# Kernel tuning notes

Measured on AMD Instinct MI355X. Metric: run time of the kernel, lower is better.

Reference implementation:

```python
import jax, jax.numpy as jnp
import numpy as np
from jax import lax

B, C, Dd, Hh, Ww = 2, 256, 8, 64, 64
E, HID, TOPK = 6, 1024, 3


def setup_inputs() -> dict:
    key = jax.random.key(0)
    ks = jax.random.split(key, 8)
    return {
        "x": jax.random.normal(ks[0], (B, C, Dd, Hh, Ww), jnp.float32),
        "attention_weights": jax.random.uniform(ks[1], (B, Dd, Hh, Ww), jnp.float32),
        "gate_w": jax.random.normal(ks[2], (E, C), jnp.float32) * 0.02,
        "gate_b": jnp.zeros((E,), jnp.float32),
        "w1": jax.random.normal(ks[3], (E, HID, C), jnp.float32) * (1.0 / np.sqrt(C)),
        "b1": jnp.zeros((E, HID), jnp.float32),
        "w2": jax.random.normal(ks[4], (E, C, HID), jnp.float32) * (1.0 / np.sqrt(HID)),
        "b2": jnp.zeros((E, C), jnp.float32),
    }


def reference(x, attention_weights, gate_w, gate_b, w1, b1, w2, b2):
    b, c, d, h, w = x.shape
    n = d * h * w
    e = gate_w.shape[0]
    xt = x.reshape(b, c, n).transpose(0, 2, 1)  # [B, N, C] tokens
    # 1x1x1 gate conv == per-voxel linear
    gv = jnp.einsum('bnc,ec->bne', xt, gate_w) + gate_b  # [B, N, E]
    gv = gv * attention_weights.reshape(b, n, 1)
    gv = jax.nn.softmax(gv, axis=-1)  # softmax over experts (dim=1 in torch layout)
    top_v, top_i = lax.top_k(gv, TOPK)  # [B, N, 3]
    # scatter top-k softmax values into a zero mask (non-topk experts get 0)
    mask = jnp.sum(jax.nn.one_hot(top_i, e, dtype=gv.dtype) * top_v[..., None], axis=-2)  # [B, N, E]
    out = jnp.zeros_like(xt)
    for ei in range(e):  # loop over small fixed expert count
        hdn = jax.nn.gelu(jnp.einsum('bnc,hc->bnh', xt, w1[ei]) + b1[ei], approximate=False)
        o = jnp.einsum('bnh,ch->bnc', hdn, w2[ei]) + b2[ei]
        out = out + mask[:, :, ei:ei + 1] * o
    return out.transpose(0, 2, 1).reshape(b, c, d, h, w)
```

## Files before the change

kernel.cpp:

```cpp
#include <hip/hip_runtime.h>
#include <hip/hip_bf16.h>
#include <math.h>

#define NN 32768
#define CC 256
#define EE 6
#define HID 1024
#define TT 64
#define NTOK 65536
#define NTILE_MAX 1044
#define NT3MAX 3078
#define NT3MAX2 1548
#define SENT 0xFFFFFFFFu

typedef __attribute__((ext_vector_type(8))) short bf16x8;
typedef __attribute__((ext_vector_type(4))) float f32x4;
typedef __attribute__((ext_vector_type(4))) unsigned int u32x4;
typedef __attribute__((ext_vector_type(2))) unsigned int u32x2;

__device__ const int CMB[20][3] = {
  {0,1,2},{0,1,3},{0,1,4},{0,1,5},{0,2,3},{0,2,4},{0,2,5},{0,3,4},{0,3,5},{0,4,5},
  {1,2,3},{1,2,4},{1,2,5},{1,3,4},{1,3,5},{1,4,5},{2,3,4},{2,3,5},{2,4,5},{3,4,5}};
__device__ const unsigned char M2B[64] = {
  255,255,255,255,255,255,255,  0,
  255,255,255,  1,255,  4, 10,255,
  255,255,255,  2,255,  5, 11,255,
  255,  7, 13,255, 16,255,255,255,
  255,255,255,  3,255,  6, 12,255,
  255,  8, 14,255, 17,255,255,255,
  255,  9, 15,255, 18,255,255,255,
   19,255,255,255,255,255,255,255};

__device__ __forceinline__ unsigned short f32_bf16(float f) {
  unsigned u = __builtin_bit_cast(unsigned, f);
  u += 0x7FFFu + ((u >> 16) & 1u);
  return (unsigned short)(u >> 16);
}

__device__ __forceinline__ unsigned cvt_pk_bf16(float lo, float hi) {
  unsigned r;
  asm("v_cvt_pk_bf16_f32 %0, %1, %2" : "=v"(r) : "v"(lo), "v"(hi));
  return r;
}

__device__ __forceinline__ float fast_gelu(float v) {
  float s = v * v;
  float a = v * -2.3021181819f;
  float m = a * 0.044715f;
  float nu = __builtin_fmaf(m, s, a);
  float z = __builtin_amdgcn_exp2f(nu);
  return v * __builtin_amdgcn_rcpf(1.0f + z);
}

__global__ void wconv(const float* __restrict__ w1, const float* __restrict__ w2,
                      unsigned short* __restrict__ w1b, unsigned short* __restrict__ w2b) {
  int i = blockIdx.x * 256 + threadIdx.x;
  w1b[i] = f32_bf16(w1[i]);
  w2b[i] = f32_bf16(w2[i]);
}


__global__ __launch_bounds__(256) void gatepack_k(
    const float* __restrict__ x, const float* __restrict__ attn,
    const float* __restrict__ gate_w, const float* __restrict__ gate_b,
    unsigned* __restrict__ setid, float* __restrict__ wsel,
    unsigned* __restrict__ ehist, unsigned char* __restrict__ Xp3) {
  __shared__ float gws[EE * CC];
  __shared__ unsigned char lx[TT * 512];
  __shared__ float gred[256 * EE];
  __shared__ unsigned hist6[EE];

  const int tid = threadIdx.x, lane = tid & 63, wv = tid >> 6;
  const int n0g = blockIdx.x * TT;
  const int bI = n0g >> 15, n0 = n0g & (NN - 1);

  for (int i = tid; i < EE * CC; i += 256) gws[i] = gate_w[i];
  if (tid < EE) hist6[tid] = 0;
  __syncthreads();

  {
    float gp[EE] = {0.f, 0.f, 0.f, 0.f, 0.f, 0.f};
    const size_t xbase = ((size_t)bI * CC + wv * 64) * NN + n0 + lane;
    #pragma unroll 1
    for (int c8 = 0; c8 < 8; ++c8) {
      float xv[8];
      #pragma unroll
      for (int j = 0; j < 8; ++j)
        xv[j] = x[xbase + (size_t)(c8 * 8 + j) * NN];
      #pragma unroll
      for (int j = 0; j < 8; ++j) {
        int c = wv * 64 + c8 * 8 + j;
        #pragma unroll
        for (int e = 0; e < EE; ++e) gp[e] = __builtin_fmaf(xv[j], gws[e * CC + c], gp[e]);
      }
      u32x4 pk;
      #pragma unroll
      for (int q = 0; q < 4; ++q) pk[q] = cvt_pk_bf16(xv[2 * q], xv[2 * q + 1]);
      *(u32x4*)(lx + lane * 512 + (wv * 64 + c8 * 8) * 2) = pk;
    }
    #pragma unroll
    for (int e = 0; e < EE; ++e) gred[(wv * 64 + lane) * EE + e] = gp[e];
  }
  __syncthreads();

  if (tid < 64) {
    float g[EE];
    #pragma unroll
    for (int e = 0; e < EE; ++e)
      g[e] = gred[(0 * 64 + tid) * EE + e] + gred[(1 * 64 + tid) * EE + e] +
             gred[(2 * 64 + tid) * EE + e] + gred[(3 * 64 + tid) * EE + e];
    float aw = attn[n0g + tid];
    float m = -1e30f;
    #pragma unroll
    for (int e = 0; e < EE; ++e) { g[e] = (g[e] + gate_b[e]) * aw; m = fmaxf(m, g[e]); }
    float ex[EE], s = 0.f;
    #pragma unroll
    for (int e = 0; e < EE; ++e) { ex[e] = expf(g[e] - m); s += ex[e]; }
    int i1 = 0; float v1 = g[0];
    #pragma unroll
    for (int e = 1; e < EE; ++e) if (g[e] > v1) { v1 = g[e]; i1 = e; }
    int i2 = -1; float v2 = -3.4e38f;
    #pragma unroll
    for (int e = 0; e < EE; ++e) if (e != i1 && g[e] > v2) { v2 = g[e]; i2 = e; }
    int i3 = -1; float v3 = -3.4e38f;
    #pragma unroll
    for (int e = 0; e < EE; ++e) if (e != i1 && e != i2 && g[e] > v3) { v3 = g[e]; i3 = e; }
    const unsigned msk = (1u << i1) | (1u << i2) | (1u << i3);
    float inv = 1.f / s;
    int slot = 0;
    #pragma unroll
    for (int e = 0; e < EE; ++e)
      if ((msk >> e) & 1u) wsel[(size_t)(n0g + tid) * 3 + (slot++)] = ex[e] * inv;
    setid[n0g + tid] = (unsigned)M2B[msk];
    atomicAdd(&hist6[i1], 1u); atomicAdd(&hist6[i2], 1u); atomicAdd(&hist6[i3], 1u);
  }
  __syncthreads();

  #pragma unroll 1
  for (int r = 0; r < 16; ++r) {
    const int t = wv * 16 + r;
    u32x2 v = *(const u32x2*)(lx + t * 512 + lane * 8);
    *(u32x2*)(Xp3 + (size_t)(n0g + t) * 512 + lane * 8) = v;
  }
  if (tid < EE) ehist[tid * 1024 + blockIdx.x] = hist6[tid];
}

__global__ __launch_bounds__(256) void prefix3_k(
    const unsigned* __restrict__ ehist, unsigned* __restrict__ ebase,
    unsigned* __restrict__ desc3, unsigned* __restrict__ tlist3,
    float* __restrict__ wp3) {
  __shared__ unsigned sc[256];
  __shared__ unsigned tot[EE], bb[EE + 1], grp[EE], tcum[EE + 1];
  const int tid = threadIdx.x;
  #pragma unroll 1
  for (int e = 0; e < EE; ++e) {
    unsigned v[4]; unsigned s = 0;
    #pragma unroll
    for (int k = 0; k < 4; ++k) { v[k] = ehist[e * 1024 + tid * 4 + k]; s += v[k]; }
    sc[tid] = s; __syncthreads();
    for (int off = 1; off < 256; off <<= 1) {
      unsigned tv = (tid >= off) ? sc[tid - off] : 0u; __syncthreads();
      sc[tid] += tv; __syncthreads();
    }
    unsigned excl = sc[tid] - s;
    if (tid == 255) tot[e] = sc[255];
    unsigned run = excl;
    #pragma unroll
    for (int k = 0; k < 4; ++k) { ebase[e * 1024 + tid * 4 + k] = run; run += v[k]; }
    __syncthreads();
  }
  if (tid == 0) {
    unsigned base = 0, tc = 0;
    for (int e = 0; e < EE; ++e) {
      bb[e] = base; tcum[e] = tc;
      unsigned gl = (tot[e] + 63) >> 6;
      grp[e] = gl;
      tc += (gl + 1) >> 1;
      base += gl << 6;
    }
    bb[EE] = base; tcum[EE] = tc;
  }
  __syncthreads();
  #pragma unroll 1
  for (int e = 0; e < EE; ++e) {
    unsigned b0 = bb[e];
    #pragma unroll
    for (int k = 0; k < 4; ++k) ebase[e * 1024 + tid * 4 + k] += b0;
  }
  if (tid < EE) {
    for (unsigned i = bb[tid] + tot[tid]; i < bb[tid + 1]; ++i) {
      tlist3[i] = SENT; wp3[i] = 0.f;
    }
  }
  __syncthreads();
  const unsigned nt = tcum[EE];
  for (int i = tid; i < NT3MAX2; i += 256) {
    unsigned d;
    if ((unsigned)i < nt) {
      int e = 0;
      while (!((unsigned)i >= tcum[e] && (unsigned)i < tcum[e + 1])) ++e;
      unsigned li = (unsigned)i - tcum[e];
      unsigned g = (bb[e] >> 6) + 2u * li;
      unsigned nh = (2u * li + 1u < grp[e]) ? 1u : 0u;
      d = ((unsigned)e << 20) | (nh << 19) | g;
    } else d = 0x3Fu << 20;
    desc3[i] = d;
  }
}

__global__ __launch_bounds__(64) void scatter3_k(
    const unsigned* __restrict__ setid, const unsigned* __restrict__ ebase,
    const float* __restrict__ wsel,
    unsigned* __restrict__ tlist3, float* __restrict__ wp3, unsigned* __restrict__ pos3) {
  const int tid = threadIdx.x;
  const int blk = blockIdx.x;
  const unsigned id = blk * 64 + tid;
  const unsigned bkt = setid[id];
  const unsigned m6 =
      (1u << CMB[bkt][0]) | (1u << CMB[bkt][1]) | (1u << CMB[bkt][2]);
  const unsigned long long below = (1ull << tid) - 1ull;
  int s = 0;
  #pragma unroll
  for (int e = 0; e < EE; ++e) {
    unsigned long long bl = __ballot((m6 >> e) & 1u);
    if ((m6 >> e) & 1u) {
      unsigned rank = (unsigned)__builtin_popcountll(bl & below);
      unsigned p = ebase[e * 1024 + blk] + rank;
      tlist3[p] = id;
      wp3[p] = wsel[(size_t)id * 3 + s];
      pos3[(size_t)id * 3 + s] = p;
      s++;
    }
  }
}

__global__ __launch_bounds__(512, 2) void moe_main3(
    const float* __restrict__ b1, const float* __restrict__ b2,
    const unsigned short* __restrict__ w1b, const unsigned short* __restrict__ w2b,
    const unsigned* __restrict__ desc3, const unsigned* __restrict__ tlist3,
    const float* __restrict__ wp3, const unsigned char* __restrict__ Xp3,
    unsigned char* __restrict__ Op3) {
  __shared__ unsigned char xs[128 * 512];
  __shared__ unsigned char hs[128 * 512];
  __shared__ unsigned tokS[128];
  __shared__ float w3S[128];

  const unsigned d = desc3[blockIdx.x];
  const unsigned e = d >> 20;
  if (e > 5) return;
  const int nh = (int)((d >> 19) & 1u);
  const int lstart = (int)(d & 0x7FFFFu) << 6;

  const int tid  = threadIdx.x;
  const int lane = tid & 63;
  const int wv   = tid >> 6;
  const int lr   = lane & 15;
  const int lg   = lane >> 4;

  if (tid < 128) {
    const int valid = (tid < 64) | nh;
    tokS[tid] = valid ? tlist3[lstart + tid] : SENT;
    w3S[tid]  = valid ? wp3[lstart + tid] : 0.f;
  }
  __syncthreads();

  {
    const int t = tid >> 2, q = tid & 3;
    unsigned tk = tokS[t];
    if (tk == SENT) tk = 0u;
    const unsigned char* src = Xp3 + (size_t)tk * 512 + q * 128;
    const unsigned tsw = ((unsigned)(t & 31)) << 4;
    #pragma unroll
    for (int i = 0; i < 8; ++i) {
      u32x4 v = *(const u32x4*)(src + i * 16);
      *(u32x4*)(xs + t * 512 + (((unsigned)(q * 128 + i * 16)) ^ tsw)) = v;
    }
  }
  __syncthreads();

  f32x4 oacc[2][8];
  #pragma unroll
  for (int fm = 0; fm < 2; ++fm)
    #pragma unroll
    for (int fn = 0; fn < 8; ++fn) oacc[fm][fn] = (f32x4){0.f, 0.f, 0.f, 0.f};

  unsigned trowA[8], tswA[8];
  #pragma unroll
  for (int fn = 0; fn < 8; ++fn) {
    int t = fn * 16 + lr;
    trowA[fn] = (unsigned)t * 512u;
    tswA[fn]  = ((unsigned)(t & 31)) << 4;
  }

  const unsigned short* w1base =
      w1b + ((size_t)(e * HID + wv * 32 + lr)) * CC + lg * 8;
  const unsigned short* w2base =
      w2b + ((size_t)(e * CC + wv * 32 + lr)) * HID + lg * 8;

  #pragma unroll 1
  for (int sc = 0; sc < 4; ++sc) {
    const unsigned short* w1c = w1base + (size_t)(sc * 256) * CC;
    const unsigned short* w2c = w2base + sc * 256;

    f32x4 hacc[2][8];
    #pragma unroll
    for (int fm = 0; fm < 2; ++fm)
      #pragma unroll
      for (int fn = 0; fn < 8; ++fn) hacc[fm][fn] = (f32x4){0.f, 0.f, 0.f, 0.f};
    #pragma unroll
    for (int ks = 0; ks < 8; ++ks) {
      bf16x8 af[2], bx[8];
      #pragma unroll
      for (int fm = 0; fm < 2; ++fm)
        af[fm] = *(const bf16x8*)(w1c + fm * 16 * CC + ks * 32);
      #pragma unroll
      for (int fn = 0; fn < 8; ++fn)
        bx[fn] = *(const bf16x8*)(xs + trowA[fn] +
                                  (((unsigned)(ks * 64 + lg * 16)) ^ tswA[fn]));
      #pragma unroll
      for (int fn = 0; fn < 8; ++fn)
        #pragma unroll
        for (int fm = 0; fm < 2; ++fm)
          hacc[fm][fn] =
              __builtin_amdgcn_mfma_f32_16x16x32_bf16(af[fm], bx[fn], hacc[fm][fn], 0, 0, 0);
    }

    {
      f32x4 b1v[2];
      #pragma unroll
      for (int fm = 0; fm < 2; ++fm)
        b1v[fm] = *(const f32x4*)&b1[e * HID + sc * 256 + wv * 32 + fm * 16 + lg * 4];
      #pragma unroll
      for (int fn = 0; fn < 8; ++fn) {
        float msk = w3S[fn * 16 + lr];
        #pragma unroll
        for (int fm = 0; fm < 2; ++fm) {
          float gg[4];
          #pragma unroll
          for (int r = 0; r < 4; ++r)
            gg[r] = fast_gelu(hacc[fm][fn][r] + b1v[fm][r]) * msk;
          u32x2 pk;
          pk[0] = cvt_pk_bf16(gg[0], gg[1]);
          pk[1] = cvt_pk_bf16(gg[2], gg[3]);
          unsigned byteo = trowA[fn] +
              (((unsigned)((wv * 32 + fm * 16 + lg * 4) * 2)) ^ tswA[fn]);
          *(u32x2*)(hs + byteo) = pk;
        }
      }
    }
    __syncthreads();

    #pragma unroll
    for (int ks = 0; ks < 8; ++ks) {
      bf16x8 am[2], bh[8];
      #pragma unroll
      for (int fm = 0; fm < 2; ++fm)
        am[fm] = *(const bf16x8*)(w2c + fm * 16 * HID + ks * 32);
      #pragma unroll
      for (int fn = 0; fn < 8; ++fn)
        bh[fn] = *(const bf16x8*)(hs + trowA[fn] +
                                  (((unsigned)(ks * 64 + lg * 16)) ^ tswA[fn]));
      #pragma unroll
      for (int fn = 0; fn < 8; ++fn)
        #pragma unroll
        for (int fm = 0; fm < 2; ++fm)
          oacc[fm][fn] =
              __builtin_amdgcn_mfma_f32_16x16x32_bf16(am[fm], bh[fn], oacc[fm][fn], 0, 0, 0);
    }
    __syncthreads();
  }

  float wt[8];
  #pragma unroll
  for (int fn = 0; fn < 8; ++fn) wt[fn] = w3S[fn * 16 + lr];
  #pragma unroll
  for (int fm = 0; fm < 2; ++fm) {
    f32x4 b2v = *(const f32x4*)&b2[e * CC + wv * 32 + fm * 16 + lg * 4];
    #pragma unroll
    for (int fn = 0; fn < 8; ++fn)
      #pragma unroll
      for (int r = 0; r < 4; ++r)
        oacc[fm][fn][r] = __builtin_fmaf(wt[fn], b2v[r], oacc[fm][fn][r]);
  }
  #pragma unroll
  for (int fn = 0; fn < 8; ++fn) {
    if (fn >= 4 && !nh) continue;
    const int row = lstart + fn * 16 + lr;
    unsigned char* po = Op3 + (size_t)row * 512;
    #pragma unroll
    for (int fm = 0; fm < 2; ++fm) {
      u32x2 pk;
      pk[0] = cvt_pk_bf16(oacc[fm][fn][0], oacc[fm][fn][1]);
      pk[1] = cvt_pk_bf16(oacc[fm][fn][2], oacc[fm][fn][3]);
      *(u32x2*)(po + (wv * 32 + fm * 16 + lg * 4) * 2) = pk;
    }
  }
}

__global__ __launch_bounds__(256) void unscatter3_k(
    const unsigned char* __restrict__ Op3, const unsigned* __restrict__ pos3,
    float* __restrict__ out) {
  __shared__ float lo[32 * 261];
  __shared__ unsigned psf[96];
  const int tid = threadIdx.x;
  const int n0g = blockIdx.x * 32;
  const int b = n0g >> 15, n0 = n0g & (NN - 1);

  if (tid < 96) psf[tid] = pos3[(size_t)n0g * 3 + tid];
  __syncthreads();

  #pragma unroll
  for (int j = 0; j < 8; ++j) {
    const int row = j * 4 + (tid >> 6);
    const int c = (tid & 63) * 4;
    float a0 = 0.f, a1 = 0.f, a2 = 0.f, a3 = 0.f;
    #pragma unroll
    for (int s = 0; s < 3; ++s) {
      const unsigned r = psf[row * 3 + s];
      u32x2 v = *(const u32x2*)(Op3 + (size_t)r * 512 + c * 2);
      a0 += __builtin_bit_cast(float, v[0] << 16);
      a1 += __builtin_bit_cast(float, v[0] & 0xFFFF0000u);
      a2 += __builtin_bit_cast(float, v[1] << 16);
      a3 += __builtin_bit_cast(float, v[1] & 0xFFFF0000u);
    }
    lo[row * 261 + c + 0] = a0; lo[row * 261 + c + 1] = a1;
    lo[row * 261 + c + 2] = a2; lo[row * 261 + c + 3] = a3;
  }
  __syncthreads();

  const int noff = tid & 31, cq = tid >> 5;
  float* po = out + (size_t)b * CC * NN + n0 + noff;
  #pragma unroll
  for (int j2 = 0; j2 < 32; ++j2) {
    int c = cq * 32 + j2;
    po[(size_t)c * NN] = lo[noff * 261 + c];
  }
}


__global__ __launch_bounds__(256) void gate_k(
    const float* __restrict__ x, const float* __restrict__ attn,
    const float* __restrict__ gate_w, const float* __restrict__ gate_b,
    unsigned* __restrict__ setid, float* __restrict__ wsel,
    unsigned* __restrict__ bhist) {
  __shared__ float gws[EE * CC];
  __shared__ unsigned hist[20];
  const int tid = threadIdx.x;
  const int blk = blockIdx.x;
  for (int i = tid; i < EE * CC; i += 256) gws[i] = gate_w[i];
  if (tid < 20) hist[tid] = 0;
  __syncthreads();

  const unsigned id = blk * 256 + tid;
  const int b = id >> 15, n = id & (NN - 1);
  const float* px = x + (size_t)b * CC * NN + n;
  float g[EE] = {0.f, 0.f, 0.f, 0.f, 0.f, 0.f};
  #pragma unroll 4
  for (int c = 0; c < CC; ++c) {
    float xv = px[(size_t)c * NN];
    #pragma unroll
    for (int e = 0; e < EE; ++e) g[e] = __builtin_fmaf(xv, gws[e * CC + c], g[e]);
  }
  float aw = attn[id];
  float m = -1e30f;
  #pragma unroll
  for (int e = 0; e < EE; ++e) { g[e] = (g[e] + gate_b[e]) * aw; m = fmaxf(m, g[e]); }
  float ex[EE], s = 0.f;
  #pragma unroll
  for (int e = 0; e < EE; ++e) { ex[e] = expf(g[e] - m); s += ex[e]; }
  int i1 = 0; float v1 = g[0];
  #pragma unroll
  for (int e = 1; e < EE; ++e) if (g[e] > v1) { v1 = g[e]; i1 = e; }
  int i2 = -1; float v2 = -3.4e38f;
  #pragma unroll
  for (int e = 0; e < EE; ++e) if (e != i1 && g[e] > v2) { v2 = g[e]; i2 = e; }
  int i3 = -1; float v3 = -3.4e38f;
  #pragma unroll
  for (int e = 0; e < EE; ++e) if (e != i1 && e != i2 && g[e] > v3) { v3 = g[e]; i3 = e; }
  const unsigned msk = (1u << i1) | (1u << i2) | (1u << i3);
  const unsigned bkt = M2B[msk];
  float inv = 1.f / s;
  int slot = 0;
  #pragma unroll
  for (int e = 0; e < EE; ++e)
    if ((msk >> e) & 1u) wsel[(size_t)id * 3 + (slot++)] = ex[e] * inv;
  setid[id] = bkt;
  atomicAdd(&hist[bkt], 1u);
  __syncthreads();
  if (tid < 20) bhist[blk * 20 + tid] = hist[tid];
}

__global__ void prefix_k(const unsigned* __restrict__ bhist, unsigned* __restrict__ bbase,
                         unsigned* __restrict__ desc) {
  __shared__ unsigned tot[20];
  __shared__ unsigned bb[21];
  __shared__ unsigned tcum[21];
  const int tid = threadIdx.x;
  if (tid < 20) {
    unsigned run = 0;
    for (int blk = 0; blk < 256; ++blk) {
      unsigned v = bhist[blk * 20 + tid];
      bbase[blk * 20 + tid] = run;
      run += v;
    }
    tot[tid] = run;
  }
  __syncthreads();
  if (tid == 0) {
    unsigned base = 0, tc = 0;
    for (int b = 0; b < 20; ++b) {
      bb[b] = base; tcum[b] = tc;
      unsigned tl = (tot[b] + 63) >> 6;
      tc += tl; base += tl << 6;
    }
    bb[20] = base; tcum[20] = tc;
  }
  __syncthreads();
  if (tid < 20) {
    unsigned b0 = bb[tid];
    for (int blk = 0; blk < 256; ++blk) bbase[blk * 20 + tid] += b0;
  }
  __syncthreads();
  const unsigned nt = tcum[20];
  for (int i = tid; i < NTILE_MAX; i += 256) {
    unsigned d;
    if ((unsigned)i < nt) {
      int b = 0;
      while (!((unsigned)i >= tcum[b] && (unsigned)i < tcum[b + 1])) ++b;
      d = ((unsigned)b << 16) | ((bb[b] >> 6) + ((unsigned)i - tcum[b]));
    } else {
      d = 0x003F0000u;
    }
    desc[i] = d;
  }
}

__global__ __launch_bounds__(256) void scatter_k(
    const unsigned* __restrict__ setid, const unsigned* __restrict__ bbase,
    const float* __restrict__ wsel,
    unsigned* __restrict__ pos, float* __restrict__ wp) {
  __shared__ unsigned wcnt[4][20];
  const int tid = threadIdx.x, lane = tid & 63, w = tid >> 6;
  const int blk = blockIdx.x;
  const unsigned id = blk * 256 + tid;
  const unsigned sid = setid[id];
  unsigned long long myb = 0;
  #pragma unroll
  for (int b = 0; b < 20; ++b) {
    unsigned long long bl = __ballot(sid == (unsigned)b);
    if (lane == 0) wcnt[w][b] = (unsigned)__builtin_popcountll(bl);
    if ((unsigned)b == sid) myb = bl;
  }
  __syncthreads();
  unsigned rank = 0;
  #pragma unroll
  for (int w2 = 0; w2 < 4; ++w2) if (w2 < w) rank += wcnt[w2][sid];
  rank += (unsigned)__builtin_popcountll(myb & ((1ull << lane) - 1ull));
  const unsigned p = bbase[blk * 20 + sid] + rank;
  pos[id] = p;
  #pragma unroll
  for (int s = 0; s < 3; ++s) wp[(size_t)p * 3 + s] = wsel[(size_t)id * 3 + s];
}

__global__ __launch_bounds__(256) void xpack_k(
    const float* __restrict__ x, const unsigned* __restrict__ pos,
    unsigned char* __restrict__ Xp) {
  __shared__ unsigned char lx[TT * 512];
  __shared__ unsigned posS[TT];
  const int tid = threadIdx.x, lane = tid & 63, wv = tid >> 6;
  const int n0g = blockIdx.x * TT;
  const int b = n0g >> 15, n0 = n0g & (NN - 1);

  if (tid < TT) posS[tid] = pos[n0g + tid];

  const float* px = x + (size_t)b * CC * NN + n0 + lane;
  #pragma unroll 1
  for (int c8 = 0; c8 < 8; ++c8) {
    float xv[8];
    #pragma unroll
    for (int j = 0; j < 8; ++j)
      xv[j] = px[(size_t)(wv * 64 + c8 * 8 + j) * NN];
    u32x4 pk;
    #pragma unroll
    for (int q = 0; q < 4; ++q) pk[q] = cvt_pk_bf16(xv[2 * q], xv[2 * q + 1]);
    *(u32x4*)(lx + lane * 512 + (wv * 64 + c8 * 8) * 2) = pk;
  }
  __syncthreads();

  #pragma unroll 1
  for (int r = 0; r < 16; ++r) {
    const int t = wv * 16 + r;
    const unsigned p = posS[t];
    u32x2 v = *(const u32x2*)(lx + t * 512 + lane * 8);
    *(u32x2*)(Xp + (size_t)p * 512 + (((unsigned)(lane * 8)) ^ (((unsigned)(p & 31)) << 4))) = v;
  }
}

__global__ __launch_bounds__(256, 2) void moe_main(
    const float* __restrict__ b1, const float* __restrict__ b2,
    const unsigned short* __restrict__ w1b, const unsigned short* __restrict__ w2b,
    const unsigned* __restrict__ desc, const float* __restrict__ wp,
    const unsigned char* __restrict__ Xp, float* __restrict__ Op) {
  __shared__ unsigned char xs[TT * CC * 2];
  __shared__ unsigned char hs[TT * 256 * 2];
  __shared__ float w3S[3 * TT];

  const unsigned d = desc[blockIdx.x];
  const unsigned bkt = d >> 16;
  if (bkt > 19) return;
  const int lstart = (int)(d & 0xFFFFu) << 6;

  const int tid  = threadIdx.x;
  const int lane = tid & 63;
  const int wv   = tid >> 6;
  const int lr   = lane & 15;
  const int lg   = lane >> 4;

  if (tid < 3 * TT) {
    int t = tid & 63, s = tid >> 6;
    w3S[s * 64 + t] = wp[(size_t)(lstart + t) * 3 + s];
  }

  {
    const unsigned char* src = Xp + (size_t)lstart * 512;
    #pragma unroll
    for (int it = 0; it < 8; ++it) {
      u32x4 v = *(const u32x4*)(src + it * 4096 + tid * 16);
      *(u32x4*)(xs + it * 4096 + tid * 16) = v;
    }
  }
  __syncthreads();

  f32x4 oacc[4][4];
  #pragma unroll
  for (int fm = 0; fm < 4; ++fm)
    #pragma unroll
    for (int fn = 0; fn < 4; ++fn) oacc[fm][fn] = (f32x4){0.f, 0.f, 0.f, 0.f};

  unsigned trowA[4], tswA[4];
  #pragma unroll
  for (int fn = 0; fn < 4; ++fn) {
    int t = fn * 16 + lr;
    trowA[fn] = (unsigned)t * 512u;
    tswA[fn]  = ((unsigned)(t & 31)) << 4;
  }

  #pragma unroll 1
  for (int xe = 0; xe < 3; ++xe) {
    const int e = CMB[bkt][xe];
    #pragma unroll 1
    for (int sc = 0; sc < 4; ++sc) {
      f32x4 hacc[4][4];
      #pragma unroll
      for (int fm = 0; fm < 4; ++fm)
        #pragma unroll
        for (int fn = 0; fn < 4; ++fn) hacc[fm][fn] = (f32x4){0.f, 0.f, 0.f, 0.f};
      const unsigned short* w1p =
          w1b + ((size_t)(e * HID + sc * 256 + wv * 64 + lr)) * CC + lg * 8;
      #pragma unroll
      for (int ks = 0; ks < 8; ++ks) {
        bf16x8 af[4], bx[4];
        #pragma unroll
        for (int fm = 0; fm < 4; ++fm)
          af[fm] = *(const bf16x8*)(w1p + fm * 16 * CC + ks * 32);
        #pragma unroll
        for (int fn = 0; fn < 4; ++fn)
          bx[fn] = *(const bf16x8*)(xs + trowA[fn] +
                                    (((unsigned)(ks * 64 + lg * 16)) ^ tswA[fn]));
        #pragma unroll
        for (int fn = 0; fn < 4; ++fn)
          #pragma unroll
          for (int fm = 0; fm < 4; ++fm)
            hacc[fm][fn] =
                __builtin_amdgcn_mfma_f32_16x16x32_bf16(af[fm], bx[fn], hacc[fm][fn], 0, 0, 0);
      }
      {
        f32x4 b1v[4];
        #pragma unroll
        for (int fm = 0; fm < 4; ++fm)
          b1v[fm] = *(const f32x4*)&b1[e * HID + sc * 256 + wv * 64 + fm * 16 + lg * 4];
        #pragma unroll
        for (int fn = 0; fn < 4; ++fn) {
          float msk = w3S[xe * 64 + fn * 16 + lr];
          #pragma unroll
          for (int fm = 0; fm < 4; ++fm) {
            float gg[4];
            #pragma unroll
            for (int r = 0; r < 4; ++r)
              gg[r] = fast_gelu(hacc[fm][fn][r] + b1v[fm][r]) * msk;
            u32x2 pk;
            pk[0] = cvt_pk_bf16(gg[0], gg[1]);
            pk[1] = cvt_pk_bf16(gg[2], gg[3]);
            unsigned byteo = trowA[fn] +
                (((unsigned)((wv * 64 + fm * 16 + lg * 4) * 2)) ^ tswA[fn]);
            *(u32x2*)(hs + byteo) = pk;
          }
        }
      }
      __syncthreads();
      const unsigned short* w2p =
          w2b + ((size_t)(e * CC + wv * 64 + lr)) * HID + sc * 256 + lg * 8;
      #pragma unroll
      for (int ks = 0; ks < 8; ++ks) {
        bf16x8 am[4], bh[4];
        #pragma unroll
        for (int fm = 0; fm < 4; ++fm)
          am[fm] = *(const bf16x8*)(w2p + fm * 16 * HID + ks * 32);
        #pragma unroll
        for (int fn = 0; fn < 4; ++fn)
          bh[fn] = *(const bf16x8*)(hs + trowA[fn] +
                                    (((unsigned)(ks * 64 + lg * 16)) ^ tswA[fn]));
        #pragma unroll
        for (int fn = 0; fn < 4; ++fn)
          #pragma unroll
          for (int fm = 0; fm < 4; ++fm)
            oacc[fm][fn] =
                __builtin_amdgcn_mfma_f32_16x16x32_bf16(am[fm], bh[fn], oacc[fm][fn], 0, 0, 0);
      }
      __syncthreads();
    }
  }

  #pragma unroll
  for (int xe = 0; xe < 3; ++xe) {
    const int e = CMB[bkt][xe];
    float msk[4];
    #pragma unroll
    for (int fn = 0; fn < 4; ++fn) msk[fn] = w3S[xe * 64 + fn * 16 + lr];
    #pragma unroll
    for (int fm = 0; fm < 4; ++fm) {
      f32x4 b2v = *(const f32x4*)&b2[e * CC + wv * 64 + fm * 16 + lg * 4];
      #pragma unroll
      for (int fn = 0; fn < 4; ++fn)
        #pragma unroll
        for (int r = 0; r < 4; ++r)
          oacc[fm][fn][r] = __builtin_fmaf(msk[fn], b2v[r], oacc[fm][fn][r]);
    }
  }
  #pragma unroll
  for (int fn = 0; fn < 4; ++fn) {
    float* po = Op + (size_t)(lstart + fn * 16 + lr) * CC;
    #pragma unroll
    for (int fm = 0; fm < 4; ++fm)
      *(f32x4*)(po + wv * 64 + fm * 16 + lg * 4) = oacc[fm][fn];
  }
}

__global__ __launch_bounds__(256) void unscatter_k(
    const float* __restrict__ Op, const unsigned* __restrict__ pos,
    float* __restrict__ out) {
  __shared__ float lo[32 * 261];
  __shared__ unsigned posS[32];
  const int tid = threadIdx.x;
  const int n0g = blockIdx.x * 32;
  const int b = n0g >> 15, n0 = n0g & (NN - 1);

  if (tid < 32) posS[tid] = pos[n0g + tid];
  __syncthreads();

  #pragma unroll
  for (int j = 0; j < 8; ++j) {
    int fidx = j * 1024 + tid * 4;
    int row = fidx >> 8, c = fidx & 255;
    f32x4 v = *(const f32x4*)(Op + (size_t)posS[row] * CC + c);
    #pragma unroll
    for (int i = 0; i < 4; ++i) lo[row * 261 + c + i] = v[i];
  }
  __syncthreads();

  const int noff = tid & 31, cq = tid >> 5;
  float* po = out + (size_t)b * CC * NN + n0 + noff;
  #pragma unroll
  for (int j2 = 0; j2 < 32; ++j2) {
    int c = cq * 32 + j2;
    po[(size_t)c * NN] = lo[noff * 261 + c];
  }
}


extern "C" void kernel_launch(void* const* d_in, const int* in_sizes, int n_in,
                              void* d_out, int out_size, void* d_ws, size_t ws_size,
                              hipStream_t stream) {
  const float* x      = (const float*)d_in[0];
  const float* attn   = (const float*)d_in[1];
  const float* gate_w = (const float*)d_in[2];
  const float* gate_b = (const float*)d_in[3];
  const float* w1     = (const float*)d_in[4];
  const float* b1     = (const float*)d_in[5];
  const float* w2     = (const float*)d_in[6];
  const float* b2     = (const float*)d_in[7];
  float* out = (float*)d_out;

  unsigned char* ws = (unsigned char*)d_ws;
  unsigned short* w1b  = (unsigned short*)(ws);
  unsigned short* w2b  = (unsigned short*)(ws + 3145728);
  unsigned*       setid= (unsigned*)(ws + 6291456);
  float*          wsel = (float*)(ws + 6553600);
  unsigned*       bhist= (unsigned*)(ws + 7340032);
  unsigned*       bbase= (unsigned*)(ws + 7360512);
  unsigned*       desc = (unsigned*)(ws + 7381120);
  unsigned*       pos  = (unsigned*)(ws + 7385344);
  float*          wp   = (float*)(ws + 7647488);
  unsigned char*  Xp   = (unsigned char*)(ws + 8449280);
  float*          Op   = (float*)(ws + 42659072);
  const size_t need_bucket = 111078656;
  unsigned*       ehist = (unsigned*)(ws + 7360512);
  unsigned*       ebase = (unsigned*)(ws + 7385088);
  unsigned*       desc3 = (unsigned*)(ws + 7409664);
  unsigned*       tlist3= (unsigned*)(ws + 7422208);
  float*          wp3   = (float*)(ws + 8210176);
  unsigned*       pos3  = (unsigned*)(ws + 8998144);
  unsigned char*  Xp3   = (unsigned char*)(ws + 9784576);
  unsigned char*  Op3   = (unsigned char*)(ws + 43339008);
  const size_t need3 = 144198912;

  wconv<<<(EE * HID * CC) / 256, 256, 0, stream>>>(w1, w2, w1b, w2b);
  if (ws_size >= need3) {
    gatepack_k<<<NTOK / TT, 256, 0, stream>>>(x, attn, gate_w, gate_b, setid, wsel, ehist, Xp3);
    prefix3_k<<<1, 256, 0, stream>>>(ehist, ebase, desc3, tlist3, wp3);
    scatter3_k<<<NTOK / 64, 64, 0, stream>>>(setid, ebase, wsel, tlist3, wp3, pos3);
    moe_main3<<<NT3MAX2, 512, 0, stream>>>(b1, b2, w1b, w2b, desc3, tlist3, wp3, Xp3, Op3);
    unscatter3_k<<<NTOK / 32, 256, 0, stream>>>(Op3, pos3, out);
  } else {
    gate_k<<<NTOK / 256, 256, 0, stream>>>(x, attn, gate_w, gate_b, setid, wsel, bhist);
    prefix_k<<<1, 256, 0, stream>>>(bhist, bbase, desc);
    scatter_k<<<NTOK / 256, 256, 0, stream>>>(setid, bbase, wsel, pos, wp);
    xpack_k<<<NTOK / TT, 256, 0, stream>>>(x, pos, Xp);
    moe_main<<<NTILE_MAX, 256, 0, stream>>>(b1, b2, w1b, w2b, desc, wp, Xp, Op);
    unscatter_k<<<NTOK / 32, 256, 0, stream>>>(Op, pos, out);
  }
}
```

Measured before the change: 522.7 us.

## Repartition MoE expert kernel so each wave owns 16 tokens end-to-end

```diff
diff --git a/kernel.cpp b/kernel.cpp
--- a/kernel.cpp
+++ b/kernel.cpp
@@ -241,7 +241,7 @@
     const float* __restrict__ wp3, const unsigned char* __restrict__ Xp3,
     unsigned char* __restrict__ Op3) {
   __shared__ unsigned char xs[128 * 512];
-  __shared__ unsigned char hs[128 * 512];
+  __shared__ unsigned char hs[8 * 8192];
   __shared__ unsigned tokS[128];
   __shared__ float w3S[128];
 
@@ -278,122 +278,89 @@
   }
   __syncthreads();
 
-  f32x4 oacc[2][8];
-  #pragma unroll
-  for (int fm = 0; fm < 2; ++fm)
-    #pragma unroll
-    for (int fn = 0; fn < 8; ++fn) oacc[fm][fn] = (f32x4){0.f, 0.f, 0.f, 0.f};
-
-  unsigned trowA[8], tswA[8];
-  #pragma unroll
-  for (int fn = 0; fn < 8; ++fn) {
-    int t = fn * 16 + lr;
-    trowA[fn] = (unsigned)t * 512u;
-    tswA[fn]  = ((unsigned)(t & 31)) << 4;
-  }
-
-  const unsigned short* w1base =
-      w1b + ((size_t)(e * HID + wv * 32 + lr)) * CC + lg * 8;
-  const unsigned short* w2base =
-      w2b + ((size_t)(e * CC + wv * 32 + lr)) * HID + lg * 8;
+  if (wv >= 4 && !nh) return;
+
+  const int myt = wv * 16 + lr;
+  const float msk = w3S[myt];
+  unsigned char* hw = hs + wv * 8192 + lr * 512;
+  const unsigned swz8 = ((unsigned)(lr & 7)) << 4;
+
+  bf16x8 bx[8];
+  {
+    const unsigned char* xrow = xs + myt * 512;
+    const unsigned tsw = ((unsigned)(myt & 31)) << 4;
+    #pragma unroll
+    for (int ks = 0; ks < 8; ++ks)
+      bx[ks] = *(const bf16x8*)(xrow + (((unsigned)(ks * 64 + lg * 16)) ^ tsw));
+  }
+
+  f32x4 oacc[16];
+  #pragma unroll
+  for (int cf = 0; cf < 16; ++cf) oacc[cf] = (f32x4){0.f, 0.f, 0.f, 0.f};
+
+  const unsigned short* w1base = w1b + ((size_t)(e * HID) + lr) * CC + lg * 8;
+  const unsigned short* w2base = w2b + ((size_t)(e * CC) + lr) * HID + lg * 8;
 
   #pragma unroll 1
   for (int sc = 0; sc < 4; ++sc) {
-    const unsigned short* w1c = w1base + (size_t)(sc * 256) * CC;
-    const unsigned short* w2c = w2base + sc * 256;
-
-    f32x4 hacc[2][8];
-    #pragma unroll
-    for (int fm = 0; fm < 2; ++fm)
-      #pragma unroll
-      for (int fn = 0; fn < 8; ++fn) hacc[fm][fn] = (f32x4){0.f, 0.f, 0.f, 0.f};
-    #pragma unroll
-    for (int ks = 0; ks < 8; ++ks) {
-      bf16x8 af[2], bx[8];
-      #pragma unroll
-      for (int fm = 0; fm < 2; ++fm)
-        af[fm] = *(const bf16x8*)(w1c + fm * 16 * CC + ks * 32);
-      #pragma unroll
-      for (int fn = 0; fn < 8; ++fn)
-        bx[fn] = *(const bf16x8*)(xs + trowA[fn] +
-                                  (((unsigned)(ks * 64 + lg * 16)) ^ tswA[fn]));
-      #pragma unroll
-      for (int fn = 0; fn < 8; ++fn)
-        #pragma unroll
-        for (int fm = 0; fm < 2; ++fm)
-          hacc[fm][fn] =
-              __builtin_amdgcn_mfma_f32_16x16x32_bf16(af[fm], bx[fn], hacc[fm][fn], 0, 0, 0);
-    }
-
+    f32x4 hacc[16];
+    #pragma unroll
+    for (int hf = 0; hf < 16; ++hf) hacc[hf] = (f32x4){0.f, 0.f, 0.f, 0.f};
     {
-      f32x4 b1v[2];
-      #pragma unroll
-      for (int fm = 0; fm < 2; ++fm)
-        b1v[fm] = *(const f32x4*)&b1[e * HID + sc * 256 + wv * 32 + fm * 16 + lg * 4];
-      #pragma unroll
-      for (int fn = 0; fn < 8; ++fn) {
-        float msk = w3S[fn * 16 + lr];
-        #pragma unroll
-        for (int fm = 0; fm < 2; ++fm) {
-          float gg[4];
-          #pragma unroll
-          for (int r = 0; r < 4; ++r)
-            gg[r] = fast_gelu(hacc[fm][fn][r] + b1v[fm][r]) * msk;
-          u32x2 pk;
-          pk[0] = cvt_pk_bf16(gg[0], gg[1]);
-          pk[1] = cvt_pk_bf16(gg[2], gg[3]);
-          unsigned byteo = trowA[fn] +
-              (((unsigned)((wv * 32 + fm * 16 + lg * 4) * 2)) ^ tswA[fn]);
-          *(u32x2*)(hs + byteo) = pk;
+      const unsigned short* w1c = w1base + (size_t)(sc * 256) * CC;
+      #pragma unroll
+      for (int ks = 0; ks < 8; ++ks) {
+        #pragma unroll
+        for (int hf = 0; hf < 16; ++hf) {
+          bf16x8 af = *(const bf16x8*)(w1c + (size_t)(hf * 16) * CC + ks * 32);
+          hacc[hf] =
+              __builtin_amdgcn_mfma_f32_16x16x32_bf16(af, bx[ks], hacc[hf], 0, 0, 0);
         }
       }
     }
-    __syncthreads();
-
-    #pragma unroll
-    for (int ks = 0; ks < 8; ++ks) {
-      bf16x8 am[2], bh[8];
-      #pragma unroll
-      for (int fm = 0; fm < 2; ++fm)
-        am[fm] = *(const bf16x8*)(w2c + fm * 16 * HID + ks * 32);
-      #pragma unroll
-      for (int fn = 0; fn < 8; ++fn)
-        bh[fn] = *(const bf16x8*)(hs + trowA[fn] +
-                                  (((unsigned)(ks * 64 + lg * 16)) ^ tswA[fn]));
-      #pragma unroll
-      for (int fn = 0; fn < 8; ++fn)
-        #pragma unroll
-        for (int fm = 0; fm < 2; ++fm)
-          oacc[fm][fn] =
-              __builtin_amdgcn_mfma_f32_16x16x32_bf16(am[fm], bh[fn], oacc[fm][fn], 0, 0, 0);
-    }
-    __syncthreads();
-  }
-
-  float wt[8];
-  #pragma unroll
-  for (int fn = 0; fn < 8; ++fn) wt[fn] = w3S[fn * 16 + lr];
-  #pragma unroll
-  for (int fm = 0; fm < 2; ++fm) {
-    f32x4 b2v = *(const f32x4*)&b2[e * CC + wv * 32 + fm * 16 + lg * 4];
-    #pragma unroll
-    for (int fn = 0; fn < 8; ++fn)
+
+    #pragma unroll
+    for (int hf = 0; hf < 16; ++hf) {
+      f32x4 b1v = *(const f32x4*)&b1[e * HID + sc * 256 + hf * 16 + lg * 4];
+      float gg[4];
       #pragma unroll
       for (int r = 0; r < 4; ++r)
-        oacc[fm][fn][r] = __builtin_fmaf(wt[fn], b2v[r], oacc[fm][fn][r]);
-  }
-  #pragma unroll
-  for (int fn = 0; fn < 8; ++fn) {
-    if (fn >= 4 && !nh) continue;
-    const int row = lstart + fn * 16 + lr;
-    unsigned char* po = Op3 + (size_t)row * 512;
-    #pragma unroll
-    for (int fm = 0; fm < 2; ++fm) {
+        gg[r] = fast_gelu(hacc[hf][r] + b1v[r]) * msk;
       u32x2 pk;
-      pk[0] = cvt_pk_bf16(oacc[fm][fn][0], oacc[fm][fn][1]);
-      pk[1] = cvt_pk_bf16(oacc[fm][fn][2], oacc[fm][fn][3]);
-      *(u32x2*)(po + (wv * 32 + fm * 16 + lg * 4) * 2) = pk;
-    }
+      pk[0] = cvt_pk_bf16(gg[0], gg[1]);
+      pk[1] = cvt_pk_bf16(gg[2], gg[3]);
+      *(u32x2*)(hw + (((unsigned)(hf * 32 + lg * 8)) ^ swz8)) = pk;
+    }
+
+    {
+      bf16x8 bh[8];
+      #pragma unroll
+      for (int ks = 0; ks < 8; ++ks)
+        bh[ks] = *(const bf16x8*)(hw + (((unsigned)(ks * 64 + lg * 16)) ^ swz8));
+      const unsigned short* w2c = w2base + sc * 256;
+      #pragma unroll
+      for (int ks = 0; ks < 8; ++ks) {
+        #pragma unroll
+        for (int cf = 0; cf < 16; ++cf) {
+          bf16x8 am = *(const bf16x8*)(w2c + (size_t)(cf * 16) * HID + ks * 32);
+          oacc[cf] =
+              __builtin_amdgcn_mfma_f32_16x16x32_bf16(am, bh[ks], oacc[cf], 0, 0, 0);
+        }
+      }
+    }
+  }
+
+  unsigned char* po = Op3 + (size_t)(lstart + myt) * 512;
+  #pragma unroll
+  for (int cf = 0; cf < 16; ++cf) {
+    f32x4 b2v = *(const f32x4*)&b2[e * CC + cf * 16 + lg * 4];
+    #pragma unroll
+    for (int r = 0; r < 4; ++r)
+      oacc[cf][r] = __builtin_fmaf(msk, b2v[r], oacc[cf][r]);
+    u32x2 pk;
+    pk[0] = cvt_pk_bf16(oacc[cf][0], oacc[cf][1]);
+    pk[1] = cvt_pk_bf16(oacc[cf][2], oacc[cf][3]);
+    *(u32x2*)(po + (cf * 16 + lg * 4) * 2) = pk;
   }
 }
 
```

Result: slower. 1.948 ms (+272.8%).
